# Kernel tuning notes

Measured on AMD Instinct MI355X. Metric: run time of the kernel, lower is better.

Reference implementation:

```python
import jax, jax.numpy as jnp
import numpy as np

N_NODES = 16384
N_EDGES = 98304
N_CAND = 1024
# GAT config from default __init__: heads=[8,8,1], features=[3,64,128,64]
LAYERS = [
    (3, 8, 64, True, True),      # (f_in, n_heads, f_out, concat, elu)
    (512, 8, 128, True, True),
    (1024, 1, 64, False, False),
]


def _gat_layer(x, src, tgt, W, a_src, a_tgt, b, skipW, nh, fo, concat, act):
    n = x.shape[0]
    proj = (x @ W).reshape(n, nh, fo)                 # [N, NH, F]
    s_src = jnp.einsum('nhf,hf->nh', proj, a_src)     # [N, NH]
    s_tgt = jnp.einsum('nhf,hf->nh', proj, a_tgt)
    e = jax.nn.leaky_relu(s_src[src] + s_tgt[tgt], 0.2)   # [E, NH]
    # numerically stable segment softmax over incoming edges of each target node
    e_max = jax.ops.segment_max(e, tgt, num_segments=n)
    ex = jnp.exp(e - jax.lax.stop_gradient(e_max)[tgt])
    denom = jax.ops.segment_sum(ex, tgt, num_segments=n)
    alpha = ex / (denom[tgt] + 1e-16)                 # [E, NH]
    agg = jax.ops.segment_sum(proj[src] * alpha[:, :, None], tgt, num_segments=n)
    out = agg + (x @ skipW).reshape(n, nh, fo)        # skip connection (projected)
    out = out.reshape(n, nh * fo) if concat else out.mean(axis=1)
    out = out + b
    return jax.nn.elu(out) if act else out


def setup_inputs() -> dict:
    key = jax.random.key(0)
    ks = iter(jax.random.split(key, 32))
    d = {}
    d['fea'] = jax.random.normal(next(ks), (N_NODES, 3), dtype=jnp.float32)
    d['edge_index'] = jax.random.randint(next(ks), (2, N_EDGES), 0, N_NODES, dtype=jnp.int32)
    d['candidates_id'] = jax.random.randint(next(ks), (N_CAND,), 0, N_NODES, dtype=jnp.int32)
    for i, (fi, nh, fo, concat, _) in enumerate(LAYERS):
        sc = 1.0 / np.sqrt(fi)
        d[f'W{i}'] = jax.random.normal(next(ks), (fi, nh * fo), dtype=jnp.float32) * sc
        d[f'a_src{i}'] = jax.random.normal(next(ks), (nh, fo), dtype=jnp.float32) * 0.1
        d[f'a_tgt{i}'] = jax.random.normal(next(ks), (nh, fo), dtype=jnp.float32) * 0.1
        d[f'b{i}'] = jnp.zeros((nh * fo if concat else fo,), dtype=jnp.float32)
        d[f'skip{i}'] = jax.random.normal(next(ks), (fi, nh * fo), dtype=jnp.float32) * sc
    # MLP head build_mlp(256, 3, 64, 1): 64->256 Tanh 256->256 Tanh 256->1
    for j, (a, bdim) in enumerate([(64, 256), (256, 256), (256, 1)], start=1):
        d[f'mW{j}'] = jax.random.normal(next(ks), (a, bdim), dtype=jnp.float32) / np.sqrt(a)
        d[f'mb{j}'] = jnp.zeros((bdim,), dtype=jnp.float32)
    return d


def reference(fea, edge_index, candidates_id,
              W0, a_src0, a_tgt0, b0, skip0,
              W1, a_src1, a_tgt1, b1, skip1,
              W2, a_src2, a_tgt2, b2, skip2,
              mW1, mb1, mW2, mb2, mW3, mb3):
    src, tgt = edge_index[0], edge_index[1]
    x = fea
    params = [(W0, a_src0, a_tgt0, b0, skip0), (W1, a_src1, a_tgt1, b1, skip1),
              (W2, a_src2, a_tgt2, b2, skip2)]
    for (fi, nh, fo, concat, act), (W, asr, atg, b, sk) in zip(LAYERS, params):
        x = _gat_layer(x, src, tgt, W, asr, atg, b, sk, nh, fo, concat, act)
    cand = x[candidates_id]                              # [C, 64]
    h = jnp.tanh(cand @ mW1 + mb1)
    h = jnp.tanh(h @ mW2 + mb2)
    prob = (h @ mW3 + mb3).squeeze(-1)                   # [C]
    return prob, candidates_id
```

## Files before the change

### kernel.cpp

```cpp
#include <hip/hip_runtime.h>
#include <cmath>

#define N_NODES 16384
#define N_EDGES 98304
#define N_CAND  1024

typedef __bf16 bf16x8 __attribute__((ext_vector_type(8)));
typedef short  s16x8  __attribute__((ext_vector_type(8)));
typedef float  f32x4  __attribute__((ext_vector_type(4)));
typedef unsigned short u16x2 __attribute__((ext_vector_type(2)));
typedef unsigned short u16x4 __attribute__((ext_vector_type(4)));

__device__ __forceinline__ unsigned short f2bf(float x) {
    unsigned u = __float_as_uint(x);
    return (unsigned short)((u + 0x7fffu + ((u >> 16) & 1u)) >> 16);
}
__device__ __forceinline__ float bf2f(unsigned short b) {
    return __uint_as_float((unsigned)b << 16);
}

#define GLL(gp, lp) __builtin_amdgcn_global_load_lds(                          \
    (const __attribute__((address_space(1))) unsigned int*)(const void*)(gp),  \
    (__attribute__((address_space(3))) unsigned int*)(void*)(lp), 16, 0, 0)

__global__ __launch_bounds__(256) void k_hist(const int* __restrict__ tgt,
                                              int* __restrict__ deg) {
    int e = blockIdx.x * 256 + threadIdx.x;
    if (e < N_EDGES) atomicAdd(&deg[tgt[e]], 1);
}

__global__ __launch_bounds__(256) void k_scan_all(const int* __restrict__ deg,
                                                  int* __restrict__ off,
                                                  int* __restrict__ cursor) {
    __shared__ int ts[256];
    int tid = threadIdx.x;
    const int4* d4 = (const int4*)(deg + tid * 64);
    int s = 0;
    #pragma unroll
    for (int i = 0; i < 16; ++i) {
        int4 v = d4[i];
        s += v.x + v.y + v.z + v.w;
    }
    ts[tid] = s;
    __syncthreads();
    for (int o = 1; o < 256; o <<= 1) {
        int t = (tid >= o) ? ts[tid - o] : 0;
        __syncthreads();
        ts[tid] += t;
        __syncthreads();
    }
    int run = ts[tid] - s;
    int4* o4 = (int4*)(off + tid * 64);
    int4* c4 = (int4*)(cursor + tid * 64);
    #pragma unroll
    for (int i = 0; i < 16; ++i) {
        int4 v = d4[i];
        int4 ov;
        ov.x = run; run += v.x;
        ov.y = run; run += v.y;
        ov.z = run; run += v.z;
        ov.w = run; run += v.w;
        o4[i] = ov;
        c4[i] = ov;
    }
    if (tid == 255) off[N_NODES] = run;
}

__global__ __launch_bounds__(256) void k_scatter(const int* __restrict__ ei,
                                                 int* __restrict__ cursor,
                                                 int* __restrict__ csrc) {
    int e = blockIdx.x * 256 + threadIdx.x;
    if (e < N_EDGES) {
        int s = ei[e];
        int t = ei[N_EDGES + e];
        int pos = atomicAdd(&cursor[t], 1);
        csrc[pos] = s;
    }
}

__global__ __launch_bounds__(256) void k_l0s(const float* __restrict__ fea,
                                             const float* __restrict__ W0,
                                             const float* __restrict__ as,
                                             const float* __restrict__ at,
                                             float* __restrict__ ssrc,
                                             float* __restrict__ stgt) {
    int n = blockIdx.x, tid = threadIdx.x;
    float f0 = fea[n * 3 + 0], f1 = fea[n * 3 + 1], f2 = fea[n * 3 + 2];
    int c1 = tid, c2 = tid + 256;
    float p1 = f0 * W0[c1] + f1 * W0[512 + c1] + f2 * W0[1024 + c1];
    float p2 = f0 * W0[c2] + f1 * W0[512 + c2] + f2 * W0[1024 + c2];
    float vs1 = p1 * as[c1], vt1 = p1 * at[c1];
    float vs2 = p2 * as[c2], vt2 = p2 * at[c2];
    #pragma unroll
    for (int o = 32; o; o >>= 1) {
        vs1 += __shfl_xor(vs1, o); vt1 += __shfl_xor(vt1, o);
        vs2 += __shfl_xor(vs2, o); vt2 += __shfl_xor(vt2, o);
    }
    int lane = tid & 63, w = tid >> 6;
    if (lane == 0) {
        ssrc[n * 8 + w]     = vs1;  stgt[n * 8 + w]     = vt1;
        ssrc[n * 8 + w + 4] = vs2;  stgt[n * 8 + w + 4] = vt2;
    }
}

__device__ __forceinline__ void pack_slot(const float* __restrict__ src0,
                                          const float* __restrict__ src1,
                                          int splitN, int NTOT, int NKB, int s,
                                          unsigned short* __restrict__ hi,
                                          unsigned short* __restrict__ lo) {
    int nb = s / (NKB * 512);
    int rem = s - nb * (NKB * 512);
    int kb = rem >> 9;
    int sl = rem & 511;
    int c = sl >> 7, n = sl & 127;
    int col = nb * 128 + n;
    const float* src;
    int cc, stride;
    if (col < splitN) { src = src0; cc = col; stride = splitN; }
    else              { src = src1; cc = col - splitN; stride = NTOT - splitN; }
    int k0 = kb * 32 + c * 8;
    s16x8 hv, lv;
    #pragma unroll
    for (int j = 0; j < 8; ++j) {
        float w = src[(size_t)(k0 + j) * stride + cc];
        unsigned short h = f2bf(w);
        hv[j] = (short)h;
        lv[j] = (short)f2bf(w - bf2f(h));
    }
    *(s16x8*)(hi + (size_t)s * 8) = hv;
    *(s16x8*)(lo + (size_t)s * 8) = lv;
}

__global__ __launch_bounds__(256) void k_pack_all(
    const float* __restrict__ W1, const float* __restrict__ sk1,
    unsigned short* __restrict__ pw1h, unsigned short* __restrict__ pw1l,
    const float* __restrict__ W2, const float* __restrict__ sk2,
    unsigned short* __restrict__ pw2h, unsigned short* __restrict__ pw2l) {
    int s = blockIdx.x * 256 + threadIdx.x;
    if (s < 131072) {
        pack_slot(W1, sk1, 1024, 2048, 16, s, pw1h, pw1l);
    } else {
        int s2 = s - 131072;
        if (s2 < 16384) pack_slot(W2, sk2, 64, 128, 32, s2, pw2h, pw2l);
    }
}

template <int F, int NTOT, int KS, bool FS>
__global__ __launch_bounds__(256, 2) void k_gemm_mfma(
    const unsigned short* __restrict__ Xhi, const unsigned short* __restrict__ Xlo,
    const unsigned short* __restrict__ Wph, const unsigned short* __restrict__ Wpl,
    float* __restrict__ out0, float* __restrict__ out1, int splitN,
    const float* __restrict__ as, const float* __restrict__ at,
    float* __restrict__ ssrc, float* __restrict__ stgt) {
    constexpr int NKB = F / 32;
    static_assert(KS == 1 || NTOT == 128, "split-K assumes single col-block");
    __shared__ unsigned short lds[2 * 16384];
    const int tid = threadIdx.x;
    const int bm  = blockIdx.y * 128;
    const int nb  = blockIdx.x;

    const int sA0 = tid, sA1 = tid + 256;
    const int rA0 = sA0 >> 2, rA1 = sA1 >> 2;
    const int cA0 = (sA0 & 3) ^ ((rA0 >> 1) & 3);
    const int cA1 = (sA1 & 3) ^ ((rA1 >> 1) & 3);
    const unsigned short* gAh0 = Xhi + (size_t)(bm + rA0) * F + cA0 * 8;
    const unsigned short* gAh1 = Xhi + (size_t)(bm + rA1) * F + cA1 * 8;
    const unsigned short* gAl0 = Xlo + (size_t)(bm + rA0) * F + cA0 * 8;
    const unsigned short* gAl1 = Xlo + (size_t)(bm + rA1) * F + cA1 * 8;
    const unsigned short* gBh  = Wph + (KS == 1 ? (size_t)nb * NKB * 4096 : 0);
    const unsigned short* gBl  = Wpl + (KS == 1 ? (size_t)nb * NKB * 4096 : 0);

    const int wave = tid >> 6, lane = tid & 63;
    const int wm = wave >> 1, wn = wave & 1;
    const int l15 = lane & 15, lc = lane >> 4;

    int offA[4], offB[4];
    #pragma unroll
    for (int mi = 0; mi < 4; ++mi) {
        int row = wm * 64 + mi * 16 + l15;
        int chp = lc ^ ((row >> 1) & 3);
        offA[mi] = row * 32 + chp * 8;
    }
    #pragma unroll
    for (int ni = 0; ni < 4; ++ni) {
        int n = wn * 64 + ni * 16 + l15;
        offB[ni] = 8192 + (lc * 128 + n) * 8;
    }

    f32x4 acc[4][4];
    #pragma unroll
    for (int i = 0; i < 4; ++i)
        #pragma unroll
        for (int j = 0; j < 4; ++j)
            acc[i][j] = (f32x4){0.f, 0.f, 0.f, 0.f};

    auto stage = [&](int kb, int buf) {
        unsigned short* l = &lds[buf * 16384];
        const size_t ka  = (size_t)kb * 32;
        const size_t kbb = (size_t)kb * 4096;
        GLL(gAh0 + ka, l + sA0 * 8);
        GLL(gAh1 + ka, l + sA1 * 8);
        GLL(gAl0 + ka, l + 4096 + sA0 * 8);
        GLL(gAl1 + ka, l + 4096 + sA1 * 8);
        GLL(gBh + kbb + sA0 * 8, l + 8192 + sA0 * 8);
        GLL(gBh + kbb + sA1 * 8, l + 8192 + sA1 * 8);
        GLL(gBl + kbb + sA0 * 8, l + 12288 + sA0 * 8);
        GLL(gBl + kbb + sA1 * 8, l + 12288 + sA1 * 8);
    };

    const int kb0 = (KS > 1) ? nb * (NKB / KS) : 0;
    const int kbN = (KS > 1) ? (NKB / KS) : NKB;

    stage(kb0, 0);
    __syncthreads();

    for (int ki = 0; ki < kbN; ++ki) {
        const int buf = ki & 1;
        if (ki + 1 < kbN) stage(kb0 + ki + 1, buf ^ 1);
        const unsigned short* l = &lds[buf * 16384];
        bf16x8 ah[4], al[4], bh[4], bl[4];
        #pragma unroll
        for (int mi = 0; mi < 4; ++mi) {
            ah[mi] = *(const bf16x8*)(l + offA[mi]);
            al[mi] = *(const bf16x8*)(l + 4096 + offA[mi]);
        }
        #pragma unroll
        for (int ni = 0; ni < 4; ++ni) {
            bh[ni] = *(const bf16x8*)(l + offB[ni]);
            bl[ni] = *(const bf16x8*)(l + 4096 + offB[ni]);
        }
        #pragma unroll
        for (int mi = 0; mi < 4; ++mi)
            #pragma unroll
            for (int ni = 0; ni < 4; ++ni) {
                acc[mi][ni] = __builtin_amdgcn_mfma_f32_16x16x32_bf16(ah[mi], bh[ni], acc[mi][ni], 0, 0, 0);
                acc[mi][ni] = __builtin_amdgcn_mfma_f32_16x16x32_bf16(ah[mi], bl[ni], acc[mi][ni], 0, 0, 0);
                acc[mi][ni] = __builtin_amdgcn_mfma_f32_16x16x32_bf16(al[mi], bh[ni], acc[mi][ni], 0, 0, 0);
            }
        __syncthreads();
    }

    if constexpr (KS > 1) {
        #pragma unroll
        for (int ni = 0; ni < 4; ++ni) {
            int col = wn * 64 + ni * 16 + l15;
            #pragma unroll
            for (int mi = 0; mi < 4; ++mi) {
                int row0 = bm + wm * 64 + mi * 16 + lc * 4;
                #pragma unroll
                for (int r = 0; r < 4; ++r)
                    out0[((size_t)nb * N_NODES + row0 + r) * NTOT + col] = acc[mi][ni][r];
            }
        }
    } else {
        #pragma unroll
        for (int ni = 0; ni < 4; ++ni) {
            int col = nb * 128 + wn * 64 + ni * 16 + l15;
            float* o;
            int cc, stride;
            if (col < splitN) { o = out0; cc = col; stride = splitN; }
            else              { o = out1; cc = col - splitN; stride = NTOT - splitN; }
            #pragma unroll
            for (int mi = 0; mi < 4; ++mi) {
                int row0 = bm + wm * 64 + mi * 16 + lc * 4;
                #pragma unroll
                for (int r = 0; r < 4; ++r)
                    o[(size_t)(row0 + r) * stride + cc] = acc[mi][ni][r];
            }
        }
        if constexpr (FS) {
            if (nb < 8) {
                float* sredS = (float*)lds;
                float* sredT = sredS + 256;
                const float* av_ = as + nb * 128;
                const float* atv = at + nb * 128;
                #pragma unroll
                for (int mi = 0; mi < 4; ++mi) {
                    #pragma unroll
                    for (int r = 0; r < 4; ++r) {
                        float ps = 0.f, pt = 0.f;
                        #pragma unroll
                        for (int ni = 0; ni < 4; ++ni) {
                            int f = wn * 64 + ni * 16 + l15;
                            float v = acc[mi][ni][r];
                            ps += v * av_[f];
                            pt += v * atv[f];
                        }
                        #pragma unroll
                        for (int o = 1; o < 16; o <<= 1) {
                            ps += __shfl_xor(ps, o);
                            pt += __shfl_xor(pt, o);
                        }
                        if (l15 == 0) {
                            int rl = wm * 64 + mi * 16 + lc * 4 + r;
                            sredS[wn * 128 + rl] = ps;
                            sredT[wn * 128 + rl] = pt;
                        }
                    }
                }
                __syncthreads();
                if (tid < 128) {
                    int row = bm + tid;
                    ssrc[row * 8 + nb] = sredS[tid] + sredS[128 + tid];
                    stgt[row * 8 + nb] = sredT[tid] + sredT[128 + tid];
                }
            }
        }
    }
}

__global__ __launch_bounds__(256) void k_red2s(const float* __restrict__ part,
                                               const float* __restrict__ as2,
                                               const float* __restrict__ at2,
                                               float* __restrict__ P2,
                                               float* __restrict__ S2,
                                               float* __restrict__ ssrc,
                                               float* __restrict__ stgt) {
    int tid = threadIdx.x;
    int node = blockIdx.x * 16 + (tid >> 4);
    int cg = tid & 15;
    int c0 = cg * 8;
    const float* p0 = part + (size_t)node * 128 + c0;
    float v[8];
    {
        float4 a = *(const float4*)(p0);
        float4 b = *(const float4*)(p0 + 4);
        v[0]=a.x; v[1]=a.y; v[2]=a.z; v[3]=a.w; v[4]=b.x; v[5]=b.y; v[6]=b.z; v[7]=b.w;
    }
    #pragma unroll
    for (int ks = 1; ks < 4; ++ks) {
        const float* pk = p0 + (size_t)ks * N_NODES * 128;
        float4 a = *(const float4*)(pk);
        float4 b = *(const float4*)(pk + 4);
        v[0]+=a.x; v[1]+=a.y; v[2]+=a.z; v[3]+=a.w; v[4]+=b.x; v[5]+=b.y; v[6]+=b.z; v[7]+=b.w;
    }
    if (cg < 8) {
        float s = 0.f, t = 0.f;
        #pragma unroll
        for (int j = 0; j < 8; ++j) {
            s += v[j] * as2[c0 + j];
            t += v[j] * at2[c0 + j];
        }
        #pragma unroll
        for (int o = 1; o < 8; o <<= 1) { s += __shfl_xor(s, o); t += __shfl_xor(t, o); }
        float* d = P2 + (size_t)node * 64 + c0;
        *(float4*)(d)     = make_float4(v[0], v[1], v[2], v[3]);
        *(float4*)(d + 4) = make_float4(v[4], v[5], v[6], v[7]);
        if (cg == 0) { ssrc[node] = s; stgt[node] = t; }
    } else {
        float* d = S2 + (size_t)node * 64 + (c0 - 64);
        *(float4*)(d)     = make_float4(v[0], v[1], v[2], v[3]);
        *(float4*)(d + 4) = make_float4(v[4], v[5], v[6], v[7]);
    }
}

__global__ __launch_bounds__(256) void k_attn0(
    const float* __restrict__ fea, const float* __restrict__ W0,
    const float* __restrict__ sk0, const float* __restrict__ ssrc,
    const float* __restrict__ stgt, const int* __restrict__ off,
    const int* __restrict__ csrc, const float* __restrict__ bias,
    unsigned short* __restrict__ ohi, unsigned short* __restrict__ olo) {
    constexpr int H = 8, K = 512;
    int n = blockIdx.x, tid = threadIdx.x;
    __shared__ float st[H], mh[H], dh[H];
    __shared__ int   srcs[256];
    __shared__ float sfea[256][3];
    __shared__ float av[256 * H];
    const int c0 = tid * 2, h0 = tid >> 5;

    float w00 = W0[c0],        w01 = W0[c0 + 1];
    float w10 = W0[512 + c0],  w11 = W0[512 + c0 + 1];
    float w20 = W0[1024 + c0], w21 = W0[1024 + c0 + 1];

    int d0 = off[n], deg = off[n + 1] - d0;
    if (tid < H) st[tid] = stgt[n * H + tid];
    __syncthreads();

    float a0 = 0.f, a1 = 0.f;

    if (deg <= 256) {
        int cnt = deg;
        if (tid < cnt) srcs[tid] = csrc[d0 + tid];
        __syncthreads();
        for (int idx = tid; idx < cnt * 3; idx += 256)
            sfea[idx / 3][idx % 3] = fea[srcs[idx / 3] * 3 + idx % 3];
        for (int idx = tid; idx < cnt * H; idx += 256) {
            int e = idx >> 3, h = idx & 7;
            float v = ssrc[srcs[e] * H + h] + st[h];
            av[idx] = (v >= 0.f) ? v : 0.2f * v;
        }
        __syncthreads();
        if (tid < H) {
            float m = -INFINITY;
            for (int e = 0; e < cnt; ++e) m = fmaxf(m, av[e * H + tid]);
            float s = 0.f;
            for (int e = 0; e < cnt; ++e) s += expf(av[e * H + tid] - m);
            mh[tid] = m;
            dh[tid] = 1.f / (s + 1e-16f);
        }
        __syncthreads();
        for (int idx = tid; idx < cnt * H; idx += 256) {
            int h = idx & 7;
            av[idx] = expf(av[idx] - mh[h]) * dh[h];
        }
        __syncthreads();
        for (int e = 0; e < cnt; ++e) {
            float al = av[e * H + h0];
            float f0 = sfea[e][0], f1 = sfea[e][1], f2 = sfea[e][2];
            a0 += (f0 * w00 + f1 * w10 + f2 * w20) * al;
            a1 += (f0 * w01 + f1 * w11 + f2 * w21) * al;
        }
    } else {
        if (tid < H) { mh[tid] = -INFINITY; dh[tid] = 0.f; }
        __syncthreads();
        for (int base = 0; base < deg; base += 256) {
            int cnt = min(256, deg - base);
            if (tid < cnt) srcs[tid] = csrc[d0 + base + tid];
            __syncthreads();
            for (int idx = tid; idx < cnt * H; idx += 256) {
                int e = idx >> 3, h = idx & 7;
                float v = ssrc[srcs[e] * H + h] + st[h];
                av[idx] = (v >= 0.f) ? v : 0.2f * v;
            }
            __syncthreads();
            if (tid < H) {
                float m = mh[tid], d = dh[tid];
                float cm = -INFINITY;
                for (int e = 0; e < cnt; ++e) cm = fmaxf(cm, av[e * H + tid]);
                float nm = fmaxf(m, cm);
                float s = 0.f;
                for (int e = 0; e < cnt; ++e) s += expf(av[e * H + tid] - nm);
                d = ((m == -INFINITY) ? 0.f : d * expf(m - nm)) + s;
                mh[tid] = nm;
                dh[tid] = d;
            }
            __syncthreads();
        }
        if (tid < H) dh[tid] = 1.f / (dh[tid] + 1e-16f);
        __syncthreads();
        for (int base = 0; base < deg; base += 256) {
            int cnt = min(256, deg - base);
            if (tid < cnt) srcs[tid] = csrc[d0 + base + tid];
            __syncthreads();
            for (int idx = tid; idx < cnt * 3; idx += 256)
                sfea[idx / 3][idx % 3] = fea[srcs[idx / 3] * 3 + idx % 3];
            for (int idx = tid; idx < cnt * H; idx += 256) {
                int e = idx >> 3, h = idx & 7;
                float v = ssrc[srcs[e] * H + h] + st[h];
                v = (v >= 0.f) ? v : 0.2f * v;
                av[idx] = expf(v - mh[h]) * dh[h];
            }
            __syncthreads();
            for (int e = 0; e < cnt; ++e) {
                float al = av[e * H + h0];
                float f0 = sfea[e][0], f1 = sfea[e][1], f2 = sfea[e][2];
                a0 += (f0 * w00 + f1 * w10 + f2 * w20) * al;
                a1 += (f0 * w01 + f1 * w11 + f2 * w21) * al;
            }
            __syncthreads();
        }
    }

    float f0 = fea[n * 3], f1 = fea[n * 3 + 1], f2 = fea[n * 3 + 2];
    float r0 = a0 + f0 * sk0[c0]     + f1 * sk0[512 + c0]     + f2 * sk0[1024 + c0]     + bias[c0];
    float r1 = a1 + f0 * sk0[c0 + 1] + f1 * sk0[512 + c0 + 1] + f2 * sk0[1024 + c0 + 1] + bias[c0 + 1];
    r0 = (r0 > 0.f) ? r0 : expm1f(r0);
    r1 = (r1 > 0.f) ? r1 : expm1f(r1);
    u16x2 hv, lv;
    unsigned short hb0 = f2bf(r0); hv[0] = hb0; lv[0] = f2bf(r0 - bf2f(hb0));
    unsigned short hb1 = f2bf(r1); hv[1] = hb1; lv[1] = f2bf(r1 - bf2f(hb1));
    *(u16x2*)(ohi + (size_t)n * K + c0) = hv;
    *(u16x2*)(olo + (size_t)n * K + c0) = lv;
}

template <int H, int FO, bool ACT, bool SPLIT, bool CAND>
__global__ __launch_bounds__(256) void k_attn_g(
    const float* __restrict__ P, const float* __restrict__ ssrc,
    const float* __restrict__ stgt, const int* __restrict__ off,
    const int* __restrict__ csrc, const float* __restrict__ bias,
    const float* __restrict__ skipin, float* __restrict__ outf,
    unsigned short* __restrict__ ohi, unsigned short* __restrict__ olo,
    const int* __restrict__ nidx) {
    constexpr int K   = H * FO;
    constexpr int VEC = (K / 256 >= 4) ? 4 : ((K / 256 >= 1) ? (K / 256) : 1);
    constexpr int NT  = K / VEC;
    int n = CAND ? nidx[blockIdx.x] : blockIdx.x;
    int orow = CAND ? blockIdx.x : n;
    int tid = threadIdx.x;
    __shared__ float st[H], mh[H], dh[H];
    __shared__ int   srcs[256];
    __shared__ float av[256 * H];

    const int c0 = (tid < NT ? tid : 0) * VEC;
    const int h0 = c0 / FO;
    const float* pc = P + c0;

    int d0 = off[n], deg = off[n + 1] - d0;
    if (tid < H) st[tid] = stgt[n * H + tid];
    __syncthreads();

    float acc[VEC];
    #pragma unroll
    for (int j = 0; j < VEC; ++j) acc[j] = 0.f;

    if (deg <= 256) {
        int cnt = deg;
        if (tid < cnt) srcs[tid] = csrc[d0 + tid];
        __syncthreads();
        for (int idx = tid; idx < cnt * H; idx += 256) {
            int e = idx / H, h = idx - (idx / H) * H;
            float v = ssrc[srcs[e] * H + h] + st[h];
            av[idx] = (v >= 0.f) ? v : 0.2f * v;
        }
        __syncthreads();
        if (tid < H) {
            float m = -INFINITY;
            for (int e = 0; e < cnt; ++e) m = fmaxf(m, av[e * H + tid]);
            float s = 0.f;
            for (int e = 0; e < cnt; ++e) s += expf(av[e * H + tid] - m);
            mh[tid] = m;
            dh[tid] = 1.f / (s + 1e-16f);
        }
        __syncthreads();
        for (int idx = tid; idx < cnt * H; idx += 256) {
            int h = idx - (idx / H) * H;
            av[idx] = expf(av[idx] - mh[h]) * dh[h];
        }
        __syncthreads();
        if (NT == 256 || tid < NT) {
            for (int e = 0; e < cnt; ++e) {
                float a = av[e * H + h0];
                if constexpr (VEC == 4) {
                    const float4 v = *(const float4*)(pc + (size_t)srcs[e] * K);
                    acc[0] += v.x * a; acc[1] += v.y * a;
                    acc[2] += v.z * a; acc[3] += v.w * a;
                } else {
                    acc[0] += pc[(size_t)srcs[e] * K] * a;
                }
            }
        }
    } else {
        if (tid < H) { mh[tid] = -INFINITY; dh[tid] = 0.f; }
        __syncthreads();
        for (int base = 0; base < deg; base += 256) {
            int cnt = min(256, deg - base);
            if (tid < cnt) srcs[tid] = csrc[d0 + base + tid];
            __syncthreads();
            for (int idx = tid; idx < cnt * H; idx += 256) {
                int e = idx / H, h = idx - (idx / H) * H;
                float v = ssrc[srcs[e] * H + h] + st[h];
                av[idx] = (v >= 0.f) ? v : 0.2f * v;
            }
            __syncthreads();
            if (tid < H) {
                float m = mh[tid], d = dh[tid];
                float cm = -INFINITY;
                for (int e = 0; e < cnt; ++e) cm = fmaxf(cm, av[e * H + tid]);
                float nm = fmaxf(m, cm);
                float s = 0.f;
                for (int e = 0; e < cnt; ++e) s += expf(av[e * H + tid] - nm);
                d = ((m == -INFINITY) ? 0.f : d * expf(m - nm)) + s;
                mh[tid] = nm;
                dh[tid] = d;
            }
            __syncthreads();
        }
        if (tid < H) dh[tid] = 1.f / (dh[tid] + 1e-16f);
        __syncthreads();
        for (int base = 0; base < deg; base += 256) {
            int cnt = min(256, deg - base);
            if (tid < cnt) srcs[tid] = csrc[d0 + base + tid];
            __syncthreads();
            for (int idx = tid; idx < cnt * H; idx += 256) {
                int e = idx / H, h = idx - (idx / H) * H;
                float v = ssrc[srcs[e] * H + h] + st[h];
                v = (v >= 0.f) ? v : 0.2f * v;
                av[idx] = expf(v - mh[h]) * dh[h];
            }
            __syncthreads();
            if (NT == 256 || tid < NT) {
                for (int e = 0; e < cnt; ++e) {
                    float a = av[e * H + h0];
                    if constexpr (VEC == 4) {
                        const float4 v = *(const float4*)(pc + (size_t)srcs[e] * K);
                        acc[0] += v.x * a; acc[1] += v.y * a;
                        acc[2] += v.z * a; acc[3] += v.w * a;
                    } else {
                        acc[0] += pc[(size_t)srcs[e] * K] * a;
                    }
                }
            }
            __syncthreads();
        }
    }

    if (NT == 256 || tid < NT) {
        float r[VEC];
        if constexpr (VEC == 4) {
            const float4 s4 = *(const float4*)(skipin + (size_t)n * K + c0);
            r[0] = acc[0] + s4.x; r[1] = acc[1] + s4.y;
            r[2] = acc[2] + s4.z; r[3] = acc[3] + s4.w;
        } else {
            r[0] = acc[0] + skipin[(size_t)n * K + c0];
        }
        #pragma unroll
        for (int j = 0; j < VEC; ++j) {
            r[j] += bias[c0 + j];
            if (ACT) r[j] = (r[j] > 0.f) ? r[j] : expm1f(r[j]);
        }
        if constexpr (SPLIT) {
            if constexpr (VEC == 4) {
                u16x4 hv, lv;
                #pragma unroll
                for (int j = 0; j < 4; ++j) {
                    unsigned short hb = f2bf(r[j]);
                    hv[j] = hb; lv[j] = f2bf(r[j] - bf2f(hb));
                }
                *(u16x4*)(ohi + (size_t)orow * K + c0) = hv;
                *(u16x4*)(olo + (size_t)orow * K + c0) = lv;
            } else {
                unsigned short hb = f2bf(r[0]);
                ohi[(size_t)orow * K + c0] = hb;
                olo[(size_t)orow * K + c0] = f2bf(r[0] - bf2f(hb));
            }
        } else {
            if constexpr (VEC == 4) {
                *(float4*)(outf + (size_t)orow * K + c0) =
                    make_float4(r[0], r[1], r[2], r[3]);
            } else {
                outf[(size_t)orow * K + c0] = r[0];
            }
        }
    }
}

__global__ __launch_bounds__(256) void k_mlp(const float* __restrict__ X3c,
                                             const int* __restrict__ cid,
                                             const float* __restrict__ W1,
                                             const float* __restrict__ b1,
                                             const float* __restrict__ W2,
                                             const float* __restrict__ b2,
                                             const float* __restrict__ W3,
                                             const float* __restrict__ b3,
                                             float* __restrict__ out) {
    __shared__ float cf[16][64];
    __shared__ float h1s[16][256];
    __shared__ float red[16][4];
    int tid = threadIdx.x;
    int cbase = blockIdx.x * 16;
    for (int i = tid; i < 16 * 64; i += 256)
        cf[i >> 6][i & 63] = X3c[(size_t)cbase * 64 + i];
    __syncthreads();
    float a[16];
    #pragma unroll
    for (int ci = 0; ci < 16; ++ci) a[ci] = b1[tid];
    for (int k = 0; k < 64; ++k) {
        float wv = W1[k * 256 + tid];
        #pragma unroll
        for (int ci = 0; ci < 16; ++ci) a[ci] += cf[ci][k] * wv;
    }
    #pragma unroll
    for (int ci = 0; ci < 16; ++ci) h1s[ci][tid] = tanhf(a[ci]);
    __syncthreads();
    #pragma unroll
    for (int ci = 0; ci < 16; ++ci) a[ci] = b2[tid];
    for (int k = 0; k < 256; ++k) {
        float wv = W2[k * 256 + tid];
        #pragma unroll
        for (int ci = 0; ci < 16; ++ci) a[ci] += h1s[ci][k] * wv;
    }
    float w3 = W3[tid];
    int lane = tid & 63, wv_ = tid >> 6;
    #pragma unroll
    for (int ci = 0; ci < 16; ++ci) {
        float v = tanhf(a[ci]) * w3;
        #pragma unroll
        for (int o = 32; o; o >>= 1) v += __shfl_xor(v, o);
        if (lane == 0) red[ci][wv_] = v;
    }
    __syncthreads();
    if (tid < 16) {
        int c = cbase + tid;
        out[c] = red[tid][0] + red[tid][1] + red[tid][2] + red[tid][3] + b3[0];
        out[N_CAND + c] = (float)cid[c];
    }
}

extern "C" void kernel_launch(void* const* d_in, const int* in_sizes, int n_in,
                              void* d_out, int out_size, void* d_ws, size_t ws_size,
                              hipStream_t stream) {
    const float* fea  = (const float*)d_in[0];
    const int*   ei   = (const int*)d_in[1];
    const int*   cid  = (const int*)d_in[2];
    const float* W0   = (const float*)d_in[3];
    const float* as0  = (const float*)d_in[4];
    const float* at0  = (const float*)d_in[5];
    const float* b0   = (const float*)d_in[6];
    const float* sk0  = (const float*)d_in[7];
    const float* W1   = (const float*)d_in[8];
    const float* as1  = (const float*)d_in[9];
    const float* at1  = (const float*)d_in[10];
    const float* b1   = (const float*)d_in[11];
    const float* sk1  = (const float*)d_in[12];
    const float* W2   = (const float*)d_in[13];
    const float* as2  = (const float*)d_in[14];
    const float* at2  = (const float*)d_in[15];
    const float* b2   = (const float*)d_in[16];
    const float* sk2  = (const float*)d_in[17];
    const float* mW1  = (const float*)d_in[18];
    const float* mb1  = (const float*)d_in[19];
    const float* mW2  = (const float*)d_in[20];
    const float* mb2  = (const float*)d_in[21];
    const float* mW3  = (const float*)d_in[22];
    const float* mb3  = (const float*)d_in[23];

    char* w = (char*)d_ws;
    auto alloc = [&](size_t bytes) -> void* {
        void* p = (void*)w;
        w += (bytes + 255) & ~(size_t)255;
        return p;
    };
    int*   deg    = (int*)alloc((size_t)N_NODES * 4);
    int*   off    = (int*)alloc((size_t)(N_NODES + 1) * 4);
    int*   cursor = (int*)alloc((size_t)N_NODES * 4);
    int*   csrc   = (int*)alloc((size_t)N_EDGES * 4);
    float* ssrc   = (float*)alloc((size_t)N_NODES * 8 * 4);
    float* stgt   = (float*)alloc((size_t)N_NODES * 8 * 4);
    float* P      = (float*)alloc((size_t)N_NODES * 1024 * 4);
    float* S      = (float*)alloc((size_t)N_NODES * 1024 * 4);
    unsigned short* Xs = (unsigned short*)alloc((size_t)N_NODES * 1024 * 4);
    unsigned short* pw1h = (unsigned short*)alloc((size_t)512 * 2048 * 2);
    unsigned short* pw1l = (unsigned short*)alloc((size_t)512 * 2048 * 2);
    unsigned short* pw2h = (unsigned short*)alloc((size_t)1024 * 128 * 2);
    unsigned short* pw2l = (unsigned short*)alloc((size_t)1024 * 128 * 2);

    unsigned short* X1hi = Xs;
    unsigned short* X1lo = Xs + (size_t)N_NODES * 512;
    unsigned short* X2hi = Xs;
    unsigned short* X2lo = Xs + (size_t)N_NODES * 1024;
    float* part = P;
    float* P2   = S;
    float* S2   = S + (size_t)N_NODES * 64;
    float* X3c  = S + (size_t)2 * N_NODES * 64;

    hipMemsetAsync(deg, 0, (size_t)N_NODES * 4, stream);
    k_hist<<<N_EDGES / 256, 256, 0, stream>>>(ei + N_EDGES, deg);
    k_scan_all<<<1, 256, 0, stream>>>(deg, off, cursor);
    k_scatter<<<N_EDGES / 256, 256, 0, stream>>>(ei, cursor, csrc);

    k_pack_all<<<576, 256, 0, stream>>>(W1, sk1, pw1h, pw1l, W2, sk2, pw2h, pw2l);

    k_l0s<<<N_NODES, 256, 0, stream>>>(fea, W0, as0, at0, ssrc, stgt);
    k_attn0<<<N_NODES, 256, 0, stream>>>(fea, W0, sk0, ssrc, stgt, off, csrc,
                                         b0, X1hi, X1lo);

    {
        dim3 g(16, N_NODES / 128);
        k_gemm_mfma<512, 2048, 1, true><<<g, 256, 0, stream>>>(
            X1hi, X1lo, pw1h, pw1l, P, S, 1024, as1, at1, ssrc, stgt);
    }
    k_attn_g<8, 128, true, true, false><<<N_NODES, 256, 0, stream>>>(
        P, ssrc, stgt, off, csrc, b1, S, nullptr, X2hi, X2lo, nullptr);

    {
        dim3 g(4, N_NODES / 128);
        k_gemm_mfma<1024, 128, 4, false><<<g, 256, 0, stream>>>(
            X2hi, X2lo, pw2h, pw2l, part, nullptr, 128,
            nullptr, nullptr, nullptr, nullptr);
    }
    k_red2s<<<N_NODES / 16, 256, 0, stream>>>(part, as2, at2, P2, S2, ssrc, stgt);
    k_attn_g<1, 64, false, false, true><<<N_CAND, 256, 0, stream>>>(
        P2, ssrc, stgt, off, csrc, b2, S2, X3c, nullptr, nullptr, cid);

    k_mlp<<<N_CAND / 16, 256, 0, stream>>>(X3c, cid, mW1, mb1, mW2, mb2, mW3, mb3,
                                           (float*)d_out);
}
```

Measured before the change: 466.7 us.

## Precompute W1·a products to compute layer-1 scores outside GEMM epilogue

Folds the attention vectors into the layer-1 weight matrix (A1 = W1·a, a 512x16 matrix) inside the packing kernel, then computes source and target scores with a separate lightweight kernel over X1. This removes the shuffle/LDS reduction epilogue from the big MFMA GEMM. The attention kernels also stop writing normalized alphas back to shared memory and instead compute exp on the fly per edge, dropping one pass and one barrier. The cost is an extra kernel launch and re-reading X1, plus recomputing exp per thread instead of once per edge-head.

```diff
diff --git a/kernel.cpp b/kernel.cpp
--- a/kernel.cpp
+++ b/kernel.cpp
@@ -10,6 +10,7 @@
 typedef float  f32x4  __attribute__((ext_vector_type(4)));
 typedef unsigned short u16x2 __attribute__((ext_vector_type(2)));
 typedef unsigned short u16x4 __attribute__((ext_vector_type(4)));
+typedef unsigned short u16x8 __attribute__((ext_vector_type(8)));
 
 __device__ __forceinline__ unsigned short f2bf(float x) {
     unsigned u = __float_as_uint(x);
@@ -135,23 +136,62 @@
     const float* __restrict__ W1, const float* __restrict__ sk1,
     unsigned short* __restrict__ pw1h, unsigned short* __restrict__ pw1l,
     const float* __restrict__ W2, const float* __restrict__ sk2,
-    unsigned short* __restrict__ pw2h, unsigned short* __restrict__ pw2l) {
+    unsigned short* __restrict__ pw2h, unsigned short* __restrict__ pw2l,
+    const float* __restrict__ as1, const float* __restrict__ at1,
+    float* __restrict__ A1) {
     int s = blockIdx.x * 256 + threadIdx.x;
     if (s < 131072) {
         pack_slot(W1, sk1, 1024, 2048, 16, s, pw1h, pw1l);
+    } else if (s < 147456) {
+        pack_slot(W2, sk2, 64, 128, 32, s - 131072, pw2h, pw2l);
     } else {
-        int s2 = s - 131072;
-        if (s2 < 16384) pack_slot(W2, sk2, 64, 128, 32, s2, pw2h, pw2l);
-    }
-}
-
-template <int F, int NTOT, int KS, bool FS>
+        int s3 = s - 147456;
+        if (s3 < 8192) {
+            int k = s3 >> 4, j = s3 & 15;
+            int h = j & 7;
+            const float* av = (j < 8) ? as1 : at1;
+            const float* wr = W1 + (size_t)k * 1024 + h * 128;
+            const float* ar = av + h * 128;
+            float acc = 0.f;
+            #pragma unroll 8
+            for (int f = 0; f < 128; ++f) acc += wr[f] * ar[f];
+            A1[k * 16 + j] = acc;
+        }
+    }
+}
+
+__global__ __launch_bounds__(256) void k_scoresA(
+    const unsigned short* __restrict__ X1hi, const unsigned short* __restrict__ X1lo,
+    const float* __restrict__ A1,
+    float* __restrict__ ssrc, float* __restrict__ stgt) {
+    int wave = threadIdx.x >> 6, lane = threadIdx.x & 63;
+    int row = blockIdx.x * 4 + wave;
+    int k0 = lane * 8;
+    u16x8 h8 = *(const u16x8*)(X1hi + (size_t)row * 512 + k0);
+    u16x8 l8 = *(const u16x8*)(X1lo + (size_t)row * 512 + k0);
+    float acc[16];
+    #pragma unroll
+    for (int j = 0; j < 16; ++j) acc[j] = 0.f;
+    #pragma unroll
+    for (int j = 0; j < 8; ++j) {
+        float x = bf2f(h8[j]) + bf2f(l8[j]);
+        const float* a = A1 + (k0 + j) * 16;
+        #pragma unroll
+        for (int jj = 0; jj < 16; ++jj) acc[jj] += x * a[jj];
+    }
+    #pragma unroll
+    for (int o = 32; o; o >>= 1)
+        #pragma unroll
+        for (int jj = 0; jj < 16; ++jj) acc[jj] += __shfl_xor(acc[jj], o);
+    if (lane < 8)       ssrc[row * 8 + lane] = acc[lane];
+    else if (lane < 16) stgt[row * 8 + (lane - 8)] = acc[lane];
+}
+
+template <int F, int NTOT, int KS>
 __global__ __launch_bounds__(256, 2) void k_gemm_mfma(
     const unsigned short* __restrict__ Xhi, const unsigned short* __restrict__ Xlo,
     const unsigned short* __restrict__ Wph, const unsigned short* __restrict__ Wpl,
-    float* __restrict__ out0, float* __restrict__ out1, int splitN,
-    const float* __restrict__ as, const float* __restrict__ at,
-    float* __restrict__ ssrc, float* __restrict__ stgt) {
+    float* __restrict__ out0, float* __restrict__ out1, int splitN) {
     constexpr int NKB = F / 32;
     static_assert(KS == 1 || NTOT == 128, "split-K assumes single col-block");
     __shared__ unsigned short lds[2 * 16384];
@@ -266,44 +306,6 @@
                 #pragma unroll
                 for (int r = 0; r < 4; ++r)
                     o[(size_t)(row0 + r) * stride + cc] = acc[mi][ni][r];
-            }
-        }
-        if constexpr (FS) {
-            if (nb < 8) {
-                float* sredS = (float*)lds;
-                float* sredT = sredS + 256;
-                const float* av_ = as + nb * 128;
-                const float* atv = at + nb * 128;
-                #pragma unroll
-                for (int mi = 0; mi < 4; ++mi) {
-                    #pragma unroll
-                    for (int r = 0; r < 4; ++r) {
-                        float ps = 0.f, pt = 0.f;
-                        #pragma unroll
-                        for (int ni = 0; ni < 4; ++ni) {
-                            int f = wn * 64 + ni * 16 + l15;
-                            float v = acc[mi][ni][r];
-                            ps += v * av_[f];
-                            pt += v * atv[f];
-                        }
-                        #pragma unroll
-                        for (int o = 1; o < 16; o <<= 1) {
-                            ps += __shfl_xor(ps, o);
-                            pt += __shfl_xor(pt, o);
-                        }
-                        if (l15 == 0) {
-                            int rl = wm * 64 + mi * 16 + lc * 4 + r;
-                            sredS[wn * 128 + rl] = ps;
-                            sredT[wn * 128 + rl] = pt;
-                        }
-                    }
-                }
-                __syncthreads();
-                if (tid < 128) {
-                    int row = bm + tid;
-                    ssrc[row * 8 + nb] = sredS[tid] + sredS[128 + tid];
-                    stgt[row * 8 + nb] = sredT[tid] + sredT[128 + tid];
-                }
             }
         }
     }
@@ -399,13 +401,9 @@
             dh[tid] = 1.f / (s + 1e-16f);
         }
         __syncthreads();
-        for (int idx = tid; idx < cnt * H; idx += 256) {
-            int h = idx & 7;
-            av[idx] = expf(av[idx] - mh[h]) * dh[h];
-        }
-        __syncthreads();
+        float mreg = mh[h0], dreg = dh[h0];
         for (int e = 0; e < cnt; ++e) {
-            float al = av[e * H + h0];
+            float al = expf(av[e * H + h0] - mreg) * dreg;
             float f0 = sfea[e][0], f1 = sfea[e][1], f2 = sfea[e][2];
             a0 += (f0 * w00 + f1 * w10 + f2 * w20) * al;
             a1 += (f0 * w01 + f1 * w11 + f2 * w21) * al;
@@ -438,6 +436,7 @@
         }
         if (tid < H) dh[tid] = 1.f / (dh[tid] + 1e-16f);
         __syncthreads();
+        float mreg = mh[h0], dreg = dh[h0];
         for (int base = 0; base < deg; base += 256) {
             int cnt = min(256, deg - base);
             if (tid < cnt) srcs[tid] = csrc[d0 + base + tid];
@@ -447,12 +446,11 @@
             for (int idx = tid; idx < cnt * H; idx += 256) {
                 int e = idx >> 3, h = idx & 7;
                 float v = ssrc[srcs[e] * H + h] + st[h];
-                v = (v >= 0.f) ? v : 0.2f * v;
-                av[idx] = expf(v - mh[h]) * dh[h];
+                av[idx] = (v >= 0.f) ? v : 0.2f * v;
             }
             __syncthreads();
             for (int e = 0; e < cnt; ++e) {
-                float al = av[e * H + h0];
+                float al = expf(av[e * H + h0] - mreg) * dreg;
                 float f0 = sfea[e][0], f1 = sfea[e][1], f2 = sfea[e][2];
                 a0 += (f0 * w00 + f1 * w10 + f2 * w20) * al;
                 a1 += (f0 * w01 + f1 * w11 + f2 * w21) * al;
@@ -522,14 +520,10 @@
             dh[tid] = 1.f / (s + 1e-16f);
         }
         __syncthreads();
-        for (int idx = tid; idx < cnt * H; idx += 256) {
-            int h = idx - (idx / H) * H;
-            av[idx] = expf(av[idx] - mh[h]) * dh[h];
-        }
-        __syncthreads();
+        float mreg = mh[h0], dreg = dh[h0];
         if (NT == 256 || tid < NT) {
             for (int e = 0; e < cnt; ++e) {
-                float a = av[e * H + h0];
+                float a = expf(av[e * H + h0] - mreg) * dreg;
                 if constexpr (VEC == 4) {
                     const float4 v = *(const float4*)(pc + (size_t)srcs[e] * K);
                     acc[0] += v.x * a; acc[1] += v.y * a;
@@ -567,6 +561,7 @@
         }
         if (tid < H) dh[tid] = 1.f / (dh[tid] + 1e-16f);
         __syncthreads();
+        float mreg = mh[h0], dreg = dh[h0];
         for (int base = 0; base < deg; base += 256) {
             int cnt = min(256, deg - base);
             if (tid < cnt) srcs[tid] = csrc[d0 + base + tid];
@@ -574,13 +569,12 @@
             for (int idx = tid; idx < cnt * H; idx += 256) {
                 int e = idx / H, h = idx - (idx / H) * H;
                 float v = ssrc[srcs[e] * H + h] + st[h];
-                v = (v >= 0.f) ? v : 0.2f * v;
-                av[idx] = expf(v - mh[h]) * dh[h];
+                av[idx] = (v >= 0.f) ? v : 0.2f * v;
             }
             __syncthreads();
             if (NT == 256 || tid < NT) {
                 for (int e = 0; e < cnt; ++e) {
-                    float a = av[e * H + h0];
+                    float a = expf(av[e * H + h0] - mreg) * dreg;
                     if constexpr (VEC == 4) {
                         const float4 v = *(const float4*)(pc + (size_t)srcs[e] * K);
                         acc[0] += v.x * a; acc[1] += v.y * a;
@@ -726,6 +720,7 @@
     int*   csrc   = (int*)alloc((size_t)N_EDGES * 4);
     float* ssrc   = (float*)alloc((size_t)N_NODES * 8 * 4);
     float* stgt   = (float*)alloc((size_t)N_NODES * 8 * 4);
+    float* A1     = (float*)alloc((size_t)512 * 16 * 4);
     float* P      = (float*)alloc((size_t)N_NODES * 1024 * 4);
     float* S      = (float*)alloc((size_t)N_NODES * 1024 * 4);
     unsigned short* Xs = (unsigned short*)alloc((size_t)N_NODES * 1024 * 4);
@@ -748,25 +743,27 @@
     k_scan_all<<<1, 256, 0, stream>>>(deg, off, cursor);
     k_scatter<<<N_EDGES / 256, 256, 0, stream>>>(ei, cursor, csrc);
 
-    k_pack_all<<<576, 256, 0, stream>>>(W1, sk1, pw1h, pw1l, W2, sk2, pw2h, pw2l);
+    k_pack_all<<<608, 256, 0, stream>>>(W1, sk1, pw1h, pw1l, W2, sk2, pw2h, pw2l,
+                                        as1, at1, A1);
 
     k_l0s<<<N_NODES, 256, 0, stream>>>(fea, W0, as0, at0, ssrc, stgt);
     k_attn0<<<N_NODES, 256, 0, stream>>>(fea, W0, sk0, ssrc, stgt, off, csrc,
                                          b0, X1hi, X1lo);
 
+    k_scoresA<<<N_NODES / 4, 256, 0, stream>>>(X1hi, X1lo, A1, ssrc, stgt);
+
     {
         dim3 g(16, N_NODES / 128);
-        k_gemm_mfma<512, 2048, 1, true><<<g, 256, 0, stream>>>(
-            X1hi, X1lo, pw1h, pw1l, P, S, 1024, as1, at1, ssrc, stgt);
+        k_gemm_mfma<512, 2048, 1><<<g, 256, 0, stream>>>(
+            X1hi, X1lo, pw1h, pw1l, P, S, 1024);
     }
     k_attn_g<8, 128, true, true, false><<<N_NODES, 256, 0, stream>>>(
         P, ssrc, stgt, off, csrc, b1, S, nullptr, X2hi, X2lo, nullptr);
 
     {
         dim3 g(4, N_NODES / 128);
-        k_gemm_mfma<1024, 128, 4, false><<<g, 256, 0, stream>>>(
-            X2hi, X2lo, pw2h, pw2l, part, nullptr, 128,
-            nullptr, nullptr, nullptr, nullptr);
+        k_gemm_mfma<1024, 128, 4><<<g, 256, 0, stream>>>(
+            X2hi, X2lo, pw2h, pw2l, part, nullptr, 128);
     }
     k_red2s<<<N_NODES / 16, 256, 0, stream>>>(part, as2, at2, P2, S2, ssrc, stgt);
     k_attn_g<1, 64, false, false, true><<<N_CAND, 256, 0, stream>>>(
```

After: 535.4 us. 14.7% more time.
